# Optimization experiments

Measured on AMD Instinct MI355X. Metric: run time of the kernel, lower is better.

The kernel has to match this reference:

```python
import jax, jax.numpy as jnp
import numpy as np

SIZE = 128
BATCH = 64
STEEPNESS = 10.0


def _odd_even_indices(n):
    """Odd-even transposition sorting network: n layers of disjoint adjacent pairs.
    All layers are padded to k = n//2 pairs with self-pairs (i,i)=(0,0), which are
    exact no-ops under the soft compare-exchange (matches pass-through wires of the
    original network)."""
    k = n // 2
    ia, ib = [], []
    for layer in range(n):
        start = layer % 2
        pa = list(range(start, n - 1, 2))
        pb = [i + 1 for i in pa]
        while len(pa) < k:  # pad with no-op self-pairs
            pa.append(0)
            pb.append(0)
        ia.append(pa)
        ib.append(pb)
    return jnp.asarray(np.array(ia, np.int32)), jnp.asarray(np.array(ib, np.int32))


def setup_inputs() -> dict:
    key = jax.random.key(0)
    return {"vectors": jax.random.normal(key, (BATCH, SIZE), dtype=jnp.float32)}


def _soft_sort(vectors):
    Bsz, n = vectors.shape
    ia, ib = _odd_even_indices(n)  # [n_layers, k] each
    x0 = vectors
    # X[b, i, j] = soft probability mass of input element i at output slot j,
    # i.e. the invariant  x[b] == vectors[b] @ X[b]  holds after every layer.
    X0 = jnp.tile(jnp.eye(n, dtype=vectors.dtype)[None], (Bsz, 1, 1))
    inv_pi = jnp.float32(1.0 / np.pi)

    def step(carry, idx):
        x, X = carry
        a_idx, b_idx = idx
        a = x[:, a_idx]  # [B, k]
        b = x[:, b_idx]  # [B, k]
        # Cauchy CDF relaxation of the comparison (module default distribution)
        alpha = jnp.arctan(STEEPNESS * (b - a)) * inv_pi + 0.5
        x = x.at[:, a_idx].set(alpha * a + (1.0 - alpha) * b)        # soft min
        x = x.at[:, b_idx].set((1.0 - alpha) * a + alpha * b)        # soft max
        A = X[:, :, a_idx]   # [B, n, k] columns feeding the 'a' wires
        Bc = X[:, :, b_idx]  # [B, n, k] columns feeding the 'b' wires
        w = alpha[:, None, :]
        X = X.at[:, :, a_idx].set(w * A + (1.0 - w) * Bc)
        X = X.at[:, :, b_idx].set((1.0 - w) * A + w * Bc)
        return (x, X), None

    (x, X), _ = jax.lax.scan(step, (x0, X0), (ia, ib))
    return x, X


def reference(vectors):
    # Returns (softly sorted values [B, n], relaxed permutation matrix [B, n, n])
    return _soft_sort(vectors)
```

## Files before the change

### kernel.cpp

```cpp
#include <hip/hip_runtime.h>
#include <math.h>

#define SIZE 128
#define BATCH 64
#define STEEP 10.0f

template<int CTRL>
__device__ __forceinline__ float dpp_mov(float x) {
    return __int_as_float(__builtin_amdgcn_update_dpp(
        __float_as_int(x), __float_as_int(x), CTRL, 0xf, 0xf, false));
}

__device__ __forceinline__ float alpha_from_delta(float delta) {
    const float C0 =  0.31830265f;
    const float C1 = -0.10587730f;
    const float C2 =  0.06160680f;
    const float C3 = -0.03706173f;
    const float C4 =  0.01676007f;
    const float C5 = -0.00373098f;
    float t   = STEEP * delta;
    float at  = fabsf(t);
    bool  inv = at > 1.0f;
    float z   = inv ? __builtin_amdgcn_rcpf(at) : at;
    float z2  = z * z;
    float q   = C5;
    q = fmaf(q, z2, C4);
    q = fmaf(q, z2, C3);
    q = fmaf(q, z2, C2);
    q = fmaf(q, z2, C1);
    q = fmaf(q, z2, C0);
    q = q * z;
    float r = inv ? 0.5f - q : q;
    return (t >= 0.0f) ? (0.5f + r) : (0.5f - r);
}

__global__ __launch_bounds__(512) void soft_sort_fused(
    const float* __restrict__ vec, float* __restrict__ out)
{
    __shared__ float alds[SIZE * 64];

    const int tid    = threadIdx.x;
    const int lane   = tid & 63;
    const int wave   = tid >> 6;
    const int batch  = blockIdx.x >> 2;
    const int rowgrp = blockIdx.x & 3;

    if (wave == 0) {
        const int c0 = 2 * lane;
        const float2 xv = *reinterpret_cast<const float2*>(vec + batch * SIZE + c0);
        float xa = xv.x, xb = xv.y;
        const bool hasR = (lane < 63);
        const bool hasL = (lane > 0);

        for (int layer = 0; layer < SIZE; layer += 2) {
            const float ae = alpha_from_delta(xb - xa);
            alds[layer * 64 + lane] = ae;
            const float t  = ae * (xa - xb);
            const float na = xb + t;
            xb = xa - t;
            xa = na;
            const float xnext = dpp_mov<0x130>(xa);
            const float ao    = alpha_from_delta(xnext - xb);
            alds[(layer + 1) * 64 + lane] = ao;
            const float aoL   = dpp_mov<0x138>(ao);
            const float xprev = dpp_mov<0x138>(xb);
            const float nxb = fmaf(ao,  xb - xnext, xnext);
            const float nxa = fmaf(aoL, xa - xprev, xprev);
            xb = hasR ? nxb : xb;
            xa = hasL ? nxa : xa;
        }
        if (rowgrp == 0)
            *reinterpret_cast<float2*>(out + batch * SIZE + c0) = make_float2(xa, xb);
    }
    __syncthreads();

    const int chunk   = lane & 15;
    const int row_sub = lane >> 4;
    const int row     = rowgrp * 32 + wave * 4 + row_sub;
    const int c8      = chunk * 8;
    const int q4      = chunk * 4;
    const int qm      = (q4 > 0) ? q4 - 1 : 0;
    const bool hasR   = (chunk < 15);
    const bool hasL   = (chunk > 0);

    float v[8];
#pragma unroll
    for (int j = 0; j < 8; ++j) v[j] = (row == c8 + j) ? 1.0f : 0.0f;

    for (int L = 0; L < 64; ++L) {
        const float4 ae = *reinterpret_cast<const float4*>(&alds[(2 * L) * 64 + q4]);
        const float4 ao = *reinterpret_cast<const float4*>(&alds[(2 * L + 1) * 64 + q4]);
        const float  aL = alds[(2 * L + 1) * 64 + qm];

        {
            float A, B, d;
            A = v[0]; B = v[1]; d = A - B; v[0] = fmaf(ae.x, d, B); v[1] = fmaf(-ae.x, d, A);
            A = v[2]; B = v[3]; d = A - B; v[2] = fmaf(ae.y, d, B); v[3] = fmaf(-ae.y, d, A);
            A = v[4]; B = v[5]; d = A - B; v[4] = fmaf(ae.z, d, B); v[5] = fmaf(-ae.z, d, A);
            A = v[6]; B = v[7]; d = A - B; v[6] = fmaf(ae.w, d, B); v[7] = fmaf(-ae.w, d, A);
        }
        const float nb0 = dpp_mov<0x101>(v[0]);
        const float pb7 = dpp_mov<0x111>(v[7]);
        {
            float A, B, d;
            A = v[1]; B = v[2]; d = A - B; v[1] = fmaf(ao.x, d, B); v[2] = fmaf(-ao.x, d, A);
            A = v[3]; B = v[4]; d = A - B; v[3] = fmaf(ao.y, d, B); v[4] = fmaf(-ao.y, d, A);
            A = v[5]; B = v[6]; d = A - B; v[5] = fmaf(ao.z, d, B); v[6] = fmaf(-ao.z, d, A);
        }
        const float r = fmaf(ao.w, v[7] - nb0, nb0);
        const float l = fmaf(aL, v[0] - pb7, pb7);
        v[7] = hasR ? r : v[7];
        v[0] = hasL ? l : v[0];
    }

    float* __restrict__ X = out + BATCH * SIZE + (batch * SIZE + row) * SIZE + c8;
    *reinterpret_cast<float4*>(X)     = make_float4(v[0], v[1], v[2], v[3]);
    *reinterpret_cast<float4*>(X + 4) = make_float4(v[4], v[5], v[6], v[7]);
}

extern "C" void kernel_launch(void* const* d_in, const int* in_sizes, int n_in,
                              void* d_out, int out_size, void* d_ws, size_t ws_size,
                              hipStream_t stream) {
    const float* vec = (const float*)d_in[0];
    float* out = (float*)d_out;
    (void)in_sizes; (void)n_in; (void)d_ws; (void)ws_size; (void)out_size;

    hipLaunchKernelGGL(soft_sort_fused, dim3(BATCH * 4), dim3(512), 0, stream,
                       vec, out);
}
```

Measured before the change: 70.50 us.

## Pipeline alpha producer wave with matrix consumer waves via double-buffered LDS

Adds a dedicated ninth producer wave that computes the comparison alphas in groups of 8 layer pairs into a double-buffered LDS ring. The eight consumer waves apply each group to the permutation-matrix rows while the producer computes the next group, instead of waiting for all 128 layers first. Boundary handling moves to alpha=1 sentinels, which removes the per-iteration selects. The arctan polynomial is also restructured with Estrin evaluation and copysign, and LDS reads are prefetched one step ahead. The cost is a block barrier per group and a larger block, and producer and consumer stay in lockstep on the shared syncs.

```diff
diff --git a/kernel.cpp b/kernel.cpp
--- a/kernel.cpp
+++ b/kernel.cpp
@@ -4,6 +4,8 @@
 #define SIZE 128
 #define BATCH 64
 #define STEEP 10.0f
+#define G 8
+#define NG 8
 
 template<int CTRL>
 __device__ __forceinline__ float dpp_mov(float x) {
@@ -18,26 +20,23 @@
     const float C3 = -0.03706173f;
     const float C4 =  0.01676007f;
     const float C5 = -0.00373098f;
-    float t   = STEEP * delta;
-    float at  = fabsf(t);
-    bool  inv = at > 1.0f;
-    float z   = inv ? __builtin_amdgcn_rcpf(at) : at;
-    float z2  = z * z;
-    float q   = C5;
-    q = fmaf(q, z2, C4);
-    q = fmaf(q, z2, C3);
-    q = fmaf(q, z2, C2);
-    q = fmaf(q, z2, C1);
-    q = fmaf(q, z2, C0);
-    q = q * z;
-    float r = inv ? 0.5f - q : q;
-    return (t >= 0.0f) ? (0.5f + r) : (0.5f - r);
+    float t  = STEEP * delta;
+    float at = fabsf(t);
+    bool inv = at > 1.0f;
+    float z  = inv ? __builtin_amdgcn_rcpf(at) : at;
+    float z2 = z * z, z4 = z2 * z2;
+    float p0 = fmaf(C1, z2, C0);
+    float p1 = fmaf(C3, z2, C2);
+    float p2 = fmaf(C5, z2, C4);
+    float q  = fmaf(fmaf(p2, z4, p1), z4, p0) * z;
+    float r  = inv ? 0.5f - q : q;
+    return 0.5f + copysignf(r, t);
 }
 
-__global__ __launch_bounds__(512) void soft_sort_fused(
+__global__ __launch_bounds__(576) void soft_sort_fused(
     const float* __restrict__ vec, float* __restrict__ out)
 {
-    __shared__ float alds[SIZE * 64];
+    __shared__ float alds[2][2 * G * 64];
 
     const int tid    = threadIdx.x;
     const int lane   = tid & 63;
@@ -45,77 +44,82 @@
     const int batch  = blockIdx.x >> 2;
     const int rowgrp = blockIdx.x & 3;
 
-    if (wave == 0) {
+    if (wave == 8) {
         const int c0 = 2 * lane;
         const float2 xv = *reinterpret_cast<const float2*>(vec + batch * SIZE + c0);
         float xa = xv.x, xb = xv.y;
         const bool hasR = (lane < 63);
         const bool hasL = (lane > 0);
 
-        for (int layer = 0; layer < SIZE; layer += 2) {
-            const float ae = alpha_from_delta(xb - xa);
-            alds[layer * 64 + lane] = ae;
-            const float t  = ae * (xa - xb);
-            const float na = xb + t;
-            xb = xa - t;
-            xa = na;
-            const float xnext = dpp_mov<0x130>(xa);
-            const float ao    = alpha_from_delta(xnext - xb);
-            alds[(layer + 1) * 64 + lane] = ao;
-            const float aoL   = dpp_mov<0x138>(ao);
-            const float xprev = dpp_mov<0x138>(xb);
-            const float nxb = fmaf(ao,  xb - xnext, xnext);
-            const float nxa = fmaf(aoL, xa - xprev, xprev);
-            xb = hasR ? nxb : xb;
-            xa = hasL ? nxa : xa;
+        for (int grp = 0; grp < NG; ++grp) {
+            float* buf = &alds[grp & 1][0];
+#pragma unroll
+            for (int j = 0; j < G; ++j) {
+                const float d  = xb - xa;
+                const float ae = alpha_from_delta(d);
+                buf[(2 * j) * 64 + lane] = ae;
+                const float nxa0 = fmaf(-ae, d, xb);
+                const float nxb0 = fmaf( ae, d, xa);
+                const float xnext = dpp_mov<0x130>(nxa0);
+                float ao = alpha_from_delta(xnext - nxb0);
+                ao = hasR ? ao : 1.0f;
+                buf[(2 * j + 1) * 64 + lane] = ao;
+                float aoL = dpp_mov<0x138>(ao);
+                aoL = hasL ? aoL : 1.0f;
+                const float xprev = dpp_mov<0x138>(nxb0);
+                xb = fmaf(ao,  nxb0 - xnext, xnext);
+                xa = fmaf(aoL, nxa0 - xprev, xprev);
+            }
+            __syncthreads();
         }
         if (rowgrp == 0)
             *reinterpret_cast<float2*>(out + batch * SIZE + c0) = make_float2(xa, xb);
+    } else {
+        const int chunk   = lane & 15;
+        const int row_sub = lane >> 4;
+        const int row     = rowgrp * 32 + wave * 4 + row_sub;
+        const int c8      = chunk * 8;
+        const int q4      = chunk * 4;
+        const int qm      = (chunk > 0) ? q4 - 1 : 63;
+
+        float v[8];
+#pragma unroll
+        for (int j = 0; j < 8; ++j) v[j] = (row == c8 + j) ? 1.0f : 0.0f;
+
+        for (int grp = 0; grp < NG; ++grp) {
+            __syncthreads();
+            const float* buf = &alds[grp & 1][0];
+            float4 ae = *reinterpret_cast<const float4*>(buf + q4);
+            float4 ao = *reinterpret_cast<const float4*>(buf + 64 + q4);
+            float  aL = buf[64 + qm];
+#pragma unroll
+            for (int j = 0; j < G; ++j) {
+                const int nj = (j < G - 1) ? j + 1 : j;
+                const float4 ae_n = *reinterpret_cast<const float4*>(buf + (2 * nj) * 64 + q4);
+                const float4 ao_n = *reinterpret_cast<const float4*>(buf + (2 * nj + 1) * 64 + q4);
+                const float  aL_n = buf[(2 * nj + 1) * 64 + qm];
+
+                float A, B, d;
+                A = v[0]; B = v[1]; d = A - B; v[0] = fmaf(ae.x, d, B); v[1] = fmaf(-ae.x, d, A);
+                A = v[2]; B = v[3]; d = A - B; v[2] = fmaf(ae.y, d, B); v[3] = fmaf(-ae.y, d, A);
+                A = v[4]; B = v[5]; d = A - B; v[4] = fmaf(ae.z, d, B); v[5] = fmaf(-ae.z, d, A);
+                A = v[6]; B = v[7]; d = A - B; v[6] = fmaf(ae.w, d, B); v[7] = fmaf(-ae.w, d, A);
+                const float nb0 = dpp_mov<0x101>(v[0]);
+                const float pb7 = dpp_mov<0x111>(v[7]);
+                A = v[1]; B = v[2]; d = A - B; v[1] = fmaf(ao.x, d, B); v[2] = fmaf(-ao.x, d, A);
+                A = v[3]; B = v[4]; d = A - B; v[3] = fmaf(ao.y, d, B); v[4] = fmaf(-ao.y, d, A);
+                A = v[5]; B = v[6]; d = A - B; v[5] = fmaf(ao.z, d, B); v[6] = fmaf(-ao.z, d, A);
+                v[7] = fmaf(ao.w, v[7] - nb0, nb0);
+                v[0] = fmaf(aL,   v[0] - pb7, pb7);
+
+                ae = ae_n; ao = ao_n; aL = aL_n;
+            }
+        }
+
+        float* __restrict__ X = out + BATCH * SIZE + (batch * SIZE + row) * SIZE + c8;
+        *reinterpret_cast<float4*>(X)     = make_float4(v[0], v[1], v[2], v[3]);
+        *reinterpret_cast<float4*>(X + 4) = make_float4(v[4], v[5], v[6], v[7]);
     }
-    __syncthreads();
-
-    const int chunk   = lane & 15;
-    const int row_sub = lane >> 4;
-    const int row     = rowgrp * 32 + wave * 4 + row_sub;
-    const int c8      = chunk * 8;
-    const int q4      = chunk * 4;
-    const int qm      = (q4 > 0) ? q4 - 1 : 0;
-    const bool hasR   = (chunk < 15);
-    const bool hasL   = (chunk > 0);
-
-    float v[8];
-#pragma unroll
-    for (int j = 0; j < 8; ++j) v[j] = (row == c8 + j) ? 1.0f : 0.0f;
-
-    for (int L = 0; L < 64; ++L) {
-        const float4 ae = *reinterpret_cast<const float4*>(&alds[(2 * L) * 64 + q4]);
-        const float4 ao = *reinterpret_cast<const float4*>(&alds[(2 * L + 1) * 64 + q4]);
-        const float  aL = alds[(2 * L + 1) * 64 + qm];
-
-        {
-            float A, B, d;
-            A = v[0]; B = v[1]; d = A - B; v[0] = fmaf(ae.x, d, B); v[1] = fmaf(-ae.x, d, A);
-            A = v[2]; B = v[3]; d = A - B; v[2] = fmaf(ae.y, d, B); v[3] = fmaf(-ae.y, d, A);
-            A = v[4]; B = v[5]; d = A - B; v[4] = fmaf(ae.z, d, B); v[5] = fmaf(-ae.z, d, A);
-            A = v[6]; B = v[7]; d = A - B; v[6] = fmaf(ae.w, d, B); v[7] = fmaf(-ae.w, d, A);
-        }
-        const float nb0 = dpp_mov<0x101>(v[0]);
-        const float pb7 = dpp_mov<0x111>(v[7]);
-        {
-            float A, B, d;
-            A = v[1]; B = v[2]; d = A - B; v[1] = fmaf(ao.x, d, B); v[2] = fmaf(-ao.x, d, A);
-            A = v[3]; B = v[4]; d = A - B; v[3] = fmaf(ao.y, d, B); v[4] = fmaf(-ao.y, d, A);
-            A = v[5]; B = v[6]; d = A - B; v[5] = fmaf(ao.z, d, B); v[6] = fmaf(-ao.z, d, A);
-        }
-        const float r = fmaf(ao.w, v[7] - nb0, nb0);
-        const float l = fmaf(aL, v[0] - pb7, pb7);
-        v[7] = hasR ? r : v[7];
-        v[0] = hasL ? l : v[0];
-    }
-
-    float* __restrict__ X = out + BATCH * SIZE + (batch * SIZE + row) * SIZE + c8;
-    *reinterpret_cast<float4*>(X)     = make_float4(v[0], v[1], v[2], v[3]);
-    *reinterpret_cast<float4*>(X + 4) = make_float4(v[4], v[5], v[6], v[7]);
 }
 
 extern "C" void kernel_launch(void* const* d_in, const int* in_sizes, int n_in,
@@ -125,6 +129,6 @@
     float* out = (float*)d_out;
     (void)in_sizes; (void)n_in; (void)d_ws; (void)ws_size; (void)out_size;
 
-    hipLaunchKernelGGL(soft_sort_fused, dim3(BATCH * 4), dim3(512), 0, stream,
+    hipLaunchKernelGGL(soft_sort_fused, dim3(BATCH * 4), dim3(576), 0, stream,
                        vec, out);
 }
```

New measurement: 69.11 us. Within noise of the previous version (-2.0%).
